# Performance work log

Measured on AMD Instinct MI355X. Metric: run time of the kernel, lower is better.

The kernel has to match this reference:

```python
import jax, jax.numpy as jnp
import numpy as np

H = 256      # hidden_channels
OUT = 128    # out_channels
NC = 20000   # central nodes
N1 = 60000   # child_cont nodes
N2 = 60000   # child_categ nodes
E = 200000   # edges per relation
B = 512      # graphs in batch
L = 2        # GNN layers
R = 4        # edge types


def seg_mean(vals, ids, n):
    s = jax.ops.segment_sum(vals, ids, num_segments=n)
    c = jax.ops.segment_sum(jnp.ones((vals.shape[0], 1), vals.dtype), ids, num_segments=n)
    return s / jnp.maximum(c, 1.0)


def setup_inputs() -> dict:
    key = jax.random.key(0)
    ks = jax.random.split(key, 24)
    nrm = lambda k, shp, s=1.0: jax.random.normal(k, shp, jnp.float32) * s

    def ei(k, ns, nd):
        k1, k2 = jax.random.split(k)
        return jnp.stack([jax.random.randint(k1, (E,), 0, ns, jnp.int32),
                          jax.random.randint(k2, (E,), 0, nd, jnp.int32)])

    inp = {
        'x_central': nrm(ks[0], (NC, 64)),
        'x_cont': nrm(ks[1], (N1, 16)),
        'x_categ': nrm(ks[2], (N2, 16)),
        'ei_c2cont': ei(ks[3], NC, N1),
        'ei_cont2c': ei(ks[4], N1, NC),
        'ei_c2categ': ei(ks[5], NC, N2),
        'ei_categ2c': ei(ks[6], N2, NC),
        'batch_central': jnp.sort(jax.random.randint(ks[7], (NC,), 0, B, jnp.int32)),
        'batch_cont': jnp.sort(jax.random.randint(ks[8], (N1,), 0, B, jnp.int32)),
        'batch_categ': jnp.sort(jax.random.randint(ks[9], (N2,), 0, B, jnp.int32)),
        'num_graphs': B,
        # input projections per node type
        'Wp_central': nrm(ks[10], (64, H), 1.0 / np.sqrt(64)),
        'bp_central': jnp.zeros((H,), jnp.float32),
        'Wp_cont': nrm(ks[11], (16, H), 0.25),
        'bp_cont': jnp.zeros((H,), jnp.float32),
        'Wp_categ': nrm(ks[12], (16, H), 0.25),
        'bp_categ': jnp.zeros((H,), jnp.float32),
        # per-layer, per-edge-type SAGEConv weights (to_hetero duplicates convs)
        'W_msg': nrm(ks[13], (L, R, H, H), 1.0 / np.sqrt(H)),
        'b_msg': jnp.zeros((L, R, H), jnp.float32),
        'W_root': nrm(ks[14], (L, R, H, H), 1.0 / np.sqrt(H)),
        # final graph linear
        'Wg': nrm(ks[15], (H, OUT), 1.0 / np.sqrt(H)),
        'bg': jnp.zeros((OUT,), jnp.float32),
    }
    return inp


def reference(x_central, x_cont, x_categ, ei_c2cont, ei_cont2c, ei_c2categ, ei_categ2c,
              batch_central, batch_cont, batch_categ, num_graphs,
              Wp_central, bp_central, Wp_cont, bp_cont, Wp_categ, bp_categ,
              W_msg, b_msg, W_root, Wg, bg):
    sizes = {'central': NC, 'child_cont': N1, 'child_categ': N2}
    x = {
        'central': x_central @ Wp_central + bp_central,
        'child_cont': x_cont @ Wp_cont + bp_cont,
        'child_categ': x_categ @ Wp_categ + bp_categ,
    }
    # (src_type, dst_type, edge_index, relation slot)
    rels = [
        ('central', 'child_cont', ei_c2cont, 0),
        ('child_cont', 'central', ei_cont2c, 1),
        ('central', 'child_categ', ei_c2categ, 2),
        ('child_categ', 'central', ei_categ2c, 3),
    ]
    n_layers = W_msg.shape[0]
    for l in range(n_layers):
        acc = {t: [] for t in x}
        for (st, dt, ei, r) in rels:
            src, dst = ei[0], ei[1]
            m = seg_mean(x[st][src], dst, sizes[dt])          # mean neighbor aggregation
            out = m @ W_msg[l, r] + b_msg[l, r] + x[dt] @ W_root[l, r]
            acc[dt].append(out)
        x = {t: jnp.mean(jnp.stack(acc[t], 0), 0) for t in acc}  # hetero aggr='mean'
        if l < n_layers - 1:
            x = {t: jax.nn.relu(v) for t, v in x.items()}
    # global mean pool per node type
    pooled = [
        seg_mean(x['central'], batch_central, num_graphs),
        seg_mean(x['child_cont'], batch_cont, num_graphs),
        seg_mean(x['child_categ'], batch_categ, num_graphs),
    ]
    graph_emb = jnp.mean(jnp.stack(pooled, 0), 0)  # 'stack' fusion
    return graph_emb @ Wg + bg
```

## Files before the change

### kernel.cpp

```cpp
#include <hip/hip_runtime.h>

#define Hh   256
#define NCn  20000
#define N1n  60000
#define N2n  60000
#define En   200000
#define Bn   512
#define OUTn 128
#define KA   96
#define PGW  1792

using bf16x8 = __attribute__((ext_vector_type(8))) __bf16;
using f32x4  = __attribute__((ext_vector_type(4))) float;
using f32x2  = __attribute__((ext_vector_type(2))) float;

__device__ __forceinline__ float bf2f(unsigned short u) {
    union { unsigned int i; float f; } v; v.i = ((unsigned int)u) << 16; return v.f;
}
__device__ __forceinline__ unsigned short f2bf(float f) {
    union { float f; unsigned int i; } v; v.f = f;
    unsigned int r = v.i + 0x7FFFu + ((v.i >> 16) & 1u);
    return (unsigned short)(r >> 16);
}
__device__ __forceinline__ int imax(int a, int b) { return a > b ? a : b; }

#if __has_builtin(__builtin_amdgcn_cvt_pk_fp8_f32) && __has_builtin(__builtin_amdgcn_cvt_pk_f32_fp8)
__device__ __forceinline__ unsigned int pack4_fp8(float v0, float v1, float v2, float v3) {
    int r = __builtin_amdgcn_cvt_pk_fp8_f32(v0, v1, 0, false);
    r = __builtin_amdgcn_cvt_pk_fp8_f32(v2, v3, r, true);
    return (unsigned int)r;
}
__device__ __forceinline__ void unpack4_fp8(unsigned int u, float& v0, float& v1, float& v2, float& v3) {
    f32x2 lo = __builtin_amdgcn_cvt_pk_f32_fp8((int)u, false);
    f32x2 hi = __builtin_amdgcn_cvt_pk_f32_fp8((int)u, true);
    v0 = lo[0]; v1 = lo[1]; v2 = hi[0]; v3 = hi[1];
}
#else
__device__ __forceinline__ unsigned char f32_to_fp8_1(float f) {
    union { float f; unsigned int i; } v; v.f = f;
    unsigned int s = (v.i >> 24) & 0x80u;
    float af = fabsf(f);
    if (!(af > 0.f)) return (unsigned char)s;
    if (af > 448.f) af = 448.f;
    v.f = af;
    int e = (int)((v.i >> 23) & 0xff) - 127;
    unsigned int m = v.i & 0x7fffffu;
    if (e < -9) return (unsigned char)s;
    if (e < -6) {
        int rb = 21 + (-6 - e) - 1;
        unsigned int man = 0x800000u | m;
        unsigned int keep = man >> (rb + 1);
        unsigned int rem = man & ((1u << (rb + 1)) - 1);
        unsigned int half = 1u << rb;
        keep += (rem > half) || (rem == half && (keep & 1));
        return (unsigned char)(s | keep);
    }
    unsigned int keep = m >> 20;
    unsigned int rem = m & 0xfffffu;
    keep += (rem > 0x80000u) || (rem == 0x80000u && (keep & 1));
    unsigned int ee = (unsigned int)(e + 7);
    if (keep == 8) { keep = 0; ee += 1; }
    if (ee >= 16) { ee = 15; keep = 6; }
    return (unsigned char)(s | (ee << 3) | keep);
}
__device__ __forceinline__ unsigned int pack4_fp8(float v0, float v1, float v2, float v3) {
    return (unsigned int)f32_to_fp8_1(v0) | ((unsigned int)f32_to_fp8_1(v1) << 8) |
           ((unsigned int)f32_to_fp8_1(v2) << 16) | ((unsigned int)f32_to_fp8_1(v3) << 24);
}
__device__ __forceinline__ float fp8_to_f32_1(unsigned int b) {
    unsigned int s = b >> 7, e = (b >> 3) & 15u, m = b & 7u;
    float v;
    if (e == 0) v = (float)m * (1.0f / 512.0f);
    else { union { unsigned int i; float f; } u; u.i = ((e + 120u) << 23) | (m << 20); v = u.f; }
    return s ? -v : v;
}
__device__ __forceinline__ void unpack4_fp8(unsigned int u, float& v0, float& v1, float& v2, float& v3) {
    v0 = fp8_to_f32_1(u & 0xffu); v1 = fp8_to_f32_1((u >> 8) & 0xffu);
    v2 = fp8_to_f32_1((u >> 16) & 0xffu); v3 = fp8_to_f32_1((u >> 24) & 0xffu);
}
#endif

struct CPtr4 { const int* p[4]; };
struct IPtr4 { int* p[4]; };
struct UPtr4 { uint2* p[4]; };

__device__ __forceinline__ float wpg_val(const float* Wm1, const float* Wr1, int k, int n) {
    int blk = k >> 8, kk = k & 255;
    float v;
    switch (blk) {
        case 0:  v = 0.5f * Wm1[1 * 65536 + kk * 256 + n]; break;
        case 1:  v = 0.5f * Wm1[3 * 65536 + kk * 256 + n]; break;
        case 2:  v = 0.5f * (Wr1[1 * 65536 + kk * 256 + n] + Wr1[3 * 65536 + kk * 256 + n]); break;
        case 3:  v = Wm1[0 * 65536 + kk * 256 + n]; break;
        case 4:  v = Wr1[0 * 65536 + kk * 256 + n]; break;
        case 5:  v = Wm1[2 * 65536 + kk * 256 + n]; break;
        default: v = Wr1[2 * 65536 + kk * 256 + n]; break;
    }
    return v * (1.0f / 3.0f);
}

#define QB0 6257
#define QB1 (QB0 + 288)
#define QB2 (QB1 + 896)
#define QB3 (QB2 + 3)
__global__ void __launch_bounds__(256) prep_mega(
        const float* __restrict__ xc, const float* __restrict__ x1, const float* __restrict__ x2,
        unsigned short* __restrict__ A0, unsigned short* __restrict__ A1,
        unsigned short* __restrict__ A2, unsigned short* __restrict__ A0c,
        unsigned short* __restrict__ xr1c, unsigned short* __restrict__ xr2c,
        int* __restrict__ deg_fill,
        const int* __restrict__ bc, const int* __restrict__ b1, const int* __restrict__ b2batch,
        int* __restrict__ bound,
        const float* __restrict__ Wm0, const float* __restrict__ Wr0,
        const float* __restrict__ bm0, const float* __restrict__ bpc,
        const float* __restrict__ bp1, const float* __restrict__ bp2,
        const float* __restrict__ Wpc, const float* __restrict__ Wp1, const float* __restrict__ Wp2,
        const float* __restrict__ Wm1, const float* __restrict__ Wr1,
        const float* __restrict__ bm1, const float* __restrict__ Wg, const float* __restrict__ bg,
        unsigned short* __restrict__ Wt3, unsigned short* __restrict__ W2t,
        float* __restrict__ bC, float* __restrict__ bB1, float* __restrict__ bB2,
        float* __restrict__ b2out) {
    __shared__ float smem[512];
    const int b = blockIdx.x, t = threadIdx.x;
    if (b < QB0) {
        const int c0 = NCn * 16, c1 = c0 + N1n * 8, c2 = c1 + N2n * 8;
        const int c3 = c2 + 320000, c4 = c3 + 3 * (Bn + 1);
        int idx = b * 256 + t;
        if (idx < c0) {
            int m = idx >> 4, c = (idx & 15) * 4;
            float4 v = *reinterpret_cast<const float4*>(xc + (size_t)m * 64 + c);
            ushort4 o = { f2bf(v.x), f2bf(v.y), f2bf(v.z), f2bf(v.w) };
            *reinterpret_cast<ushort4*>(A0 + (size_t)m * KA + c) = o;
            *reinterpret_cast<ushort4*>(A0c + (size_t)m * 64 + c) = o;
        } else if (idx < c2) {
            bool is1 = idx < c1;
            int i = idx - (is1 ? c0 : c1);
            int m = i >> 3, c = (i & 7) * 4;
            const float* x = is1 ? x1 : x2;
            unsigned short* A = is1 ? A1 : A2;
            unsigned short* xr = is1 ? xr1c : xr2c;
            ushort4 o = { 0, 0, 0, 0 };
            if (c < 16) {
                float4 v = *reinterpret_cast<const float4*>(x + (size_t)m * 16 + c);
                o.x = f2bf(v.x); o.y = f2bf(v.y); o.z = f2bf(v.z); o.w = f2bf(v.w);
                *reinterpret_cast<ushort4*>(xr + (size_t)m * 16 + c) = o;
            }
            *reinterpret_cast<ushort4*>(A + (size_t)m * KA + 64 + c) = o;
        } else if (idx < c3) {
            deg_fill[idx - c2] = 0;
        } else if (idx < c4) {
            int i4 = idx - c3;
            int ty = i4 / (Bn + 1); int bb = i4 - ty * (Bn + 1);
            const int* batch = (ty == 0) ? bc : (ty == 1) ? b1 : b2batch;
            int n = (ty == 0) ? NCn : (ty == 1) ? N1n : N2n;
            int lo = 0, hi = n;
            while (lo < hi) { int mid = (lo + hi) >> 1; if (batch[mid] < bb) lo = mid + 1; else hi = mid; }
            bound[i4] = lo;
        }
    } else if (b < QB1) {
        int bi = b - QB0;
        int mat = bi / 96, k = bi - mat * 96;
        int n = t;
        float acc = 0.f;
        if (k < 64) {
            const float* wp = Wpc + k * 256;
            if (mat == 0) {
#pragma unroll 8
                for (int j = 0; j < 256; ++j)
                    acc = fmaf(wp[j], 0.5f * (Wr0[1 * 65536 + j * 256 + n] + Wr0[3 * 65536 + j * 256 + n]), acc);
            } else if (mat == 1) {
#pragma unroll 8
                for (int j = 0; j < 256; ++j)
                    acc = fmaf(wp[j], Wm0[0 * 65536 + j * 256 + n], acc);
            } else {
#pragma unroll 8
                for (int j = 0; j < 256; ++j)
                    acc = fmaf(wp[j], Wm0[2 * 65536 + j * 256 + n], acc);
            }
        } else if (k < 80) {
            int kk = k - 64;
            if (mat == 0) {
                const float* wp = Wp1 + kk * 256;
#pragma unroll 8
                for (int j = 0; j < 256; ++j)
                    acc = fmaf(wp[j], 0.5f * Wm0[1 * 65536 + j * 256 + n], acc);
            } else if (mat == 1) {
                const float* wp = Wp1 + kk * 256;
#pragma unroll 8
                for (int j = 0; j < 256; ++j)
                    acc = fmaf(wp[j], Wr0[0 * 65536 + j * 256 + n], acc);
            } else {
                const float* wp = Wp2 + kk * 256;
#pragma unroll 8
                for (int j = 0; j < 256; ++j)
                    acc = fmaf(wp[j], Wr0[2 * 65536 + j * 256 + n], acc);
            }
        } else {
            if (mat == 0) {
                const float* wp = Wp2 + (k - 80) * 256;
#pragma unroll 8
                for (int j = 0; j < 256; ++j)
                    acc = fmaf(wp[j], 0.5f * Wm0[3 * 65536 + j * 256 + n], acc);
            }
        }
        Wt3[(size_t)mat * 256 * KA + n * KA + k] = f2bf(acc);
    } else if (b < QB2) {
        int kb = b - QB1;
        int k0 = kb * 2, k1 = k0 + 1;
        float* v0 = smem;
        float* v1 = smem + 256;
        v0[t] = wpg_val(Wm1, Wr1, k0, t);
        v1[t] = wpg_val(Wm1, Wr1, k1, t);
        __syncthreads();
        int o = t & 127;
        const float* vv = (t < 128) ? v0 : v1;
        int kk = (t < 128) ? k0 : k1;
        float acc = 0.f;
        for (int n = 0; n < 256; ++n) acc = fmaf(vv[n], Wg[n * OUTn + o], acc);
        W2t[(size_t)o * PGW + kk] = f2bf(acc);
    } else if (b < QB3) {
        int which = b - QB2;
        int n = t;
        if (which == 0) {
            float s0 = 0, s1 = 0, s2 = 0;
#pragma unroll 4
            for (int j = 0; j < 256; ++j) {
                float wr1 = Wr0[1 * 65536 + j * 256 + n], wr3 = Wr0[3 * 65536 + j * 256 + n];
                float wm1 = Wm0[1 * 65536 + j * 256 + n], wm3 = Wm0[3 * 65536 + j * 256 + n];
                s0 = fmaf(bpc[j], 0.5f * (wr1 + wr3), s0);
                s1 = fmaf(bp1[j], 0.5f * wm1, s1);
                s2 = fmaf(bp2[j], 0.5f * wm3, s2);
            }
            bC[n] = s0 + s1 + s2 + 0.5f * (bm0[1 * 256 + n] + bm0[3 * 256 + n]);
        } else if (which == 1) {
            float t0 = 0, t1 = 0;
#pragma unroll 4
            for (int j = 0; j < 256; ++j) {
                t0 = fmaf(bpc[j], Wm0[0 * 65536 + j * 256 + n], t0);
                t1 = fmaf(bp1[j], Wr0[0 * 65536 + j * 256 + n], t1);
            }
            bB1[n] = t0 + t1 + bm0[0 * 256 + n];
        } else {
            float u0 = 0, u1 = 0;
#pragma unroll 4
            for (int j = 0; j < 256; ++j) {
                u0 = fmaf(bpc[j], Wm0[2 * 65536 + j * 256 + n], u0);
                u1 = fmaf(bp2[j], Wr0[2 * 65536 + j * 256 + n], u1);
            }
            bB2[n] = u0 + u1 + bm0[2 * 256 + n];
        }
    } else {
        const float third = 1.0f / 3.0f;
        smem[t] = third * (0.5f * (bm1[1 * 256 + t] + bm1[3 * 256 + t]) +
                           bm1[0 * 256 + t] + bm1[2 * 256 + t]);
        __syncthreads();
        if (t < OUTn) {
            float acc = bg[t];
            for (int n = 0; n < 256; ++n) acc = fmaf(smem[n], Wg[n * OUTn + t], acc);
            b2out[t] = acc;
        }
    }
}

__device__ __forceinline__ int degoff_of(int rel) {
    const int t[4] = { 0, N1n, N1n + NCn, N1n + NCn + N2n };
    return t[rel];
}
__device__ __forceinline__ int nrel_of(int rel) {
    const int t[4] = { N1n, NCn, N2n, NCn };
    return t[rel];
}
__device__ __forceinline__ void rel_chunk(int b, int& rel, int& c) {
    if (b < 59)       { rel = 0; c = b; }
    else if (b < 79)  { rel = 1; c = b - 59; }
    else if (b < 138) { rel = 2; c = b - 79; }
    else              { rel = 3; c = b - 138; }
}
__global__ void deg_count_all(CPtr4 dst, int* __restrict__ deg_all) {
    int i = blockIdx.x * 256 + threadIdx.x;
    if (i >= 4 * En) return;
    int rel = i / En; int e = i - rel * En;
    atomicAdd(&deg_all[degoff_of(rel) + dst.p[rel][e]], 1);
}
__global__ void __launch_bounds__(1024) scan_chunk_all(const int* __restrict__ deg_all,
                                                       IPtr4 rp, int* __restrict__ partials) {
    int rel, c; rel_chunk(blockIdx.x, rel, c);
    int n = nrel_of(rel);
    __shared__ int sh[1024];
    int tid = threadIdx.x;
    int i = c * 1024 + tid;
    int v = (i < n) ? deg_all[degoff_of(rel) + i] : 0;
    sh[tid] = v; __syncthreads();
    for (int off = 1; off < 1024; off <<= 1) {
        int t = (tid >= off) ? sh[tid - off] : 0; __syncthreads();
        sh[tid] += t; __syncthreads();
    }
    if (i < n) rp.p[rel][i] = sh[tid] - v;
    if (tid == 1023) partials[rel * 64 + c] = sh[1023];
}
__global__ void scan_partials_all(int* partials) {
    const int nch[4] = { 59, 20, 59, 20 };
    int rel = blockIdx.x;
    __shared__ int sh[64];
    int tid = threadIdx.x;
    int v = (tid < nch[rel]) ? partials[rel * 64 + tid] : 0;
    sh[tid] = v; __syncthreads();
    for (int off = 1; off < 64; off <<= 1) {
        int t = (tid >= off) ? sh[tid - off] : 0; __syncthreads();
        sh[tid] += t; __syncthreads();
    }
    if (tid < nch[rel]) partials[rel * 64 + tid] = sh[tid] - v;
}
__global__ void __launch_bounds__(1024) scan_add_all(IPtr4 rp, const int* __restrict__ partials) {
    int rel, c; rel_chunk(blockIdx.x, rel, c);
    int n = nrel_of(rel);
    int tid = threadIdx.x;
    int i = c * 1024 + tid;
    if (i < n) rp.p[rel][i] += partials[rel * 64 + c];
    if (c == 0 && tid == 0) rp.p[rel][n] = En;
}
__global__ void scatter_all(CPtr4 src, CPtr4 dst, CPtr4 rp, int* fill_all, UPtr4 pay) {
    int i = blockIdx.x * 256 + threadIdx.x;
    if (i >= 4 * En) return;
    int rel = i / En; int e = i - rel * En;
    int d = dst.p[rel][e];
    int rb = rp.p[rel][d];
    int deg = rp.p[rel][d + 1] - rb;
    float w = 1.0f / (float)imax(deg, 1);
    int pos = rb + atomicAdd(&fill_all[degoff_of(rel) + d], 1);
    pay.p[rel][pos] = make_uint2((unsigned int)src.p[rel][e], __float_as_uint(w));
}

struct RawDesc {
    const unsigned short* feat;
    const int* rowptr;
    const uint2* pay;
    unsigned short* out;
    int fstride;
    int sh;
    int n_dst;
    int ocol;
};
__global__ void raw_agg(RawDesc d0, RawDesc d1, RawDesc d2, RawDesc d3) {
    RawDesc d = (blockIdx.y == 0) ? d0 : (blockIdx.y == 1) ? d1 : (blockIdx.y == 2) ? d2 : d3;
    int idx = blockIdx.x * 256 + threadIdx.x;
    int node = idx >> d.sh;
    int c4 = idx & ((1 << d.sh) - 1);
    if (node >= d.n_dst) return;
    int s = d.rowptr[node], e = d.rowptr[node + 1];
    float a0 = 0.f, a1 = 0.f, a2 = 0.f, a3 = 0.f;
    float b0 = 0.f, b1 = 0.f, b2 = 0.f, b3 = 0.f;
    int i = s;
    for (; i + 1 < e; i += 2) {
        int sc1 = (int)d.pay[i].x, sc2 = (int)d.pay[i + 1].x;
        ushort4 v1 = *reinterpret_cast<const ushort4*>(d.feat + (size_t)sc1 * d.fstride + c4 * 4);
        ushort4 v2 = *reinterpret_cast<const ushort4*>(d.feat + (size_t)sc2 * d.fstride + c4 * 4);
        a0 += bf2f(v1.x); a1 += bf2f(v1.y); a2 += bf2f(v1.z); a3 += bf2f(v1.w);
        b0 += bf2f(v2.x); b1 += bf2f(v2.y); b2 += bf2f(v2.z); b3 += bf2f(v2.w);
    }
    if (i < e) {
        int sc1 = (int)d.pay[i].x;
        ushort4 v1 = *reinterpret_cast<const ushort4*>(d.feat + (size_t)sc1 * d.fstride + c4 * 4);
        a0 += bf2f(v1.x); a1 += bf2f(v1.y); a2 += bf2f(v1.z); a3 += bf2f(v1.w);
    }
    a0 += b0; a1 += b1; a2 += b2; a3 += b3;
    float inv = 1.0f / (float)imax(e - s, 1);
    ushort4 o;
    o.x = f2bf(a0 * inv); o.y = f2bf(a1 * inv); o.z = f2bf(a2 * inv); o.w = f2bf(a3 * inv);
    *reinterpret_cast<ushort4*>(d.out + (size_t)node * KA + d.ocol + c4 * 4) = o;
}

struct G96 {
    const unsigned short* A;
    const unsigned short* Wt;
    const float* bias;
    unsigned char* C;
    int M;
};
__global__ void __launch_bounds__(256) gemm96(G96 g0, G96 g1, G96 g2) {
    G96 g = (blockIdx.y == 0) ? g0 : (blockIdx.y == 1) ? g1 : g2;
    const int m0 = blockIdx.x * 32;
    if (m0 >= g.M) return;
    const int tid = threadIdx.x;
    const int wid = tid >> 6, lane = tid & 63;
    const int llo = lane & 15, lhi = lane >> 4;
    const int cb = wid * 64;

    const unsigned short* pA[2];
#pragma unroll
    for (int rt = 0; rt < 2; ++rt)
        pA[rt] = g.A + (size_t)(m0 + rt * 16 + llo) * KA + lhi * 8;
    const unsigned short* pB[4];
#pragma unroll
    for (int ct = 0; ct < 4; ++ct)
        pB[ct] = g.Wt + (size_t)(cb + ct * 16 + llo) * KA + lhi * 8;

    f32x4 acc[2][4] = {};
    bf16x8 a0[2], a1[2], a2[2], b0[4], b1[4], b2[4];
#pragma unroll
    for (int t = 0; t < 2; ++t) {
        a0[t] = *reinterpret_cast<const bf16x8*>(pA[t]);
        a1[t] = *reinterpret_cast<const bf16x8*>(pA[t] + 32);
        a2[t] = *reinterpret_cast<const bf16x8*>(pA[t] + 64);
    }
#pragma unroll
    for (int t = 0; t < 4; ++t) {
        b0[t] = *reinterpret_cast<const bf16x8*>(pB[t]);
        b1[t] = *reinterpret_cast<const bf16x8*>(pB[t] + 32);
        b2[t] = *reinterpret_cast<const bf16x8*>(pB[t] + 64);
    }
#pragma unroll
    for (int rt = 0; rt < 2; ++rt)
#pragma unroll
        for (int ct = 0; ct < 4; ++ct) {
            acc[rt][ct] = __builtin_amdgcn_mfma_f32_16x16x32_bf16(b0[ct], a0[rt], acc[rt][ct], 0, 0, 0);
            acc[rt][ct] = __builtin_amdgcn_mfma_f32_16x16x32_bf16(b1[ct], a1[rt], acc[rt][ct], 0, 0, 0);
            acc[rt][ct] = __builtin_amdgcn_mfma_f32_16x16x32_bf16(b2[ct], a2[rt], acc[rt][ct], 0, 0, 0);
        }

#pragma unroll
    for (int rt = 0; rt < 2; ++rt) {
        const int row = m0 + rt * 16 + llo;
#pragma unroll
        for (int ct = 0; ct < 4; ++ct) {
            const int col0 = cb + ct * 16 + lhi * 4;
            float4 bv = *reinterpret_cast<const float4*>(g.bias + col0);
            float v0 = fmaxf(acc[rt][ct][0] + bv.x, 0.f);
            float v1 = fmaxf(acc[rt][ct][1] + bv.y, 0.f);
            float v2 = fmaxf(acc[rt][ct][2] + bv.z, 0.f);
            float v3 = fmaxf(acc[rt][ct][3] + bv.w, 0.f);
            unsigned int o = pack4_fp8(v0, v1, v2, v3);
            *reinterpret_cast<unsigned int*>(g.C + (size_t)row * 256 + col0) = o;
        }
    }
}

struct PDesc {
    const unsigned char* feat;
    const int* bound;
    const int* rowptr;
    const uint2* pay;
};
struct PAll { PDesc d[7]; };
__global__ void __launch_bounds__(256) pg_all(PAll all, float* __restrict__ part) {
    PDesc d = all.d[blockIdx.y];
    const int g = blockIdx.x, z = blockIdx.z;
    const int tid = threadIdx.x, wid = tid >> 6, lane = tid & 63;
    const int ns = d.bound[g], ne = d.bound[g + 1];
    float r0 = 0.f, r1 = 0.f, r2 = 0.f, r3 = 0.f;
    if (d.rowptr) {
        const int es = d.rowptr[ns], ee = d.rowptr[ne];
        const int len = ee - es;
        const int s = es + ((len * z) >> 2), e = es + ((len * (z + 1)) >> 2);
        float a[4][4] = {};
        for (int i = s + wid * 8; i < e; i += 32) {
            uint2 p[8]; float w[8];
#pragma unroll
            for (int j = 0; j < 8; ++j) {
                int ij = i + j;
                bool ok = ij < e;
                p[j] = d.pay[ok ? ij : (e - 1)];
                w[j] = ok ? __uint_as_float(p[j].y) : 0.f;
            }
            unsigned int u[8];
#pragma unroll
            for (int j = 0; j < 8; ++j)
                u[j] = *reinterpret_cast<const unsigned int*>(
                    d.feat + (size_t)p[j].x * 256 + lane * 4);
#pragma unroll
            for (int j = 0; j < 8; ++j) {
                float f0, f1, f2, f3;
                unpack4_fp8(u[j], f0, f1, f2, f3);
                int q = j & 3;
                a[q][0] = fmaf(f0, w[j], a[q][0]);
                a[q][1] = fmaf(f1, w[j], a[q][1]);
                a[q][2] = fmaf(f2, w[j], a[q][2]);
                a[q][3] = fmaf(f3, w[j], a[q][3]);
            }
        }
        r0 = (a[0][0] + a[1][0]) + (a[2][0] + a[3][0]);
        r1 = (a[0][1] + a[1][1]) + (a[2][1] + a[3][1]);
        r2 = (a[0][2] + a[1][2]) + (a[2][2] + a[3][2]);
        r3 = (a[0][3] + a[1][3]) + (a[2][3] + a[3][3]);
    } else {
        const int len = ne - ns;
        const int s = ns + ((len * z) >> 2), e = ns + ((len * (z + 1)) >> 2);
        float a[4][4] = {};
        for (int n = s + wid * 4; n < e; n += 16) {
            unsigned int u[4];
#pragma unroll
            for (int j = 0; j < 4; ++j) {
                int nj = n + j;
                bool ok = nj < e;
                u[j] = ok ? *reinterpret_cast<const unsigned int*>(
                                d.feat + (size_t)nj * 256 + lane * 4) : 0u;
            }
#pragma unroll
            for (int j = 0; j < 4; ++j) {
                float f0, f1, f2, f3;
                unpack4_fp8(u[j], f0, f1, f2, f3);
                a[j][0] += f0; a[j][1] += f1; a[j][2] += f2; a[j][3] += f3;
            }
        }
        r0 = (a[0][0] + a[1][0]) + (a[2][0] + a[3][0]);
        r1 = (a[0][1] + a[1][1]) + (a[2][1] + a[3][1]);
        r2 = (a[0][2] + a[1][2]) + (a[2][2] + a[3][2]);
        r3 = (a[0][3] + a[1][3]) + (a[2][3] + a[3][3]);
    }
    __shared__ float sh[4][256];
    sh[wid][lane * 4 + 0] = r0; sh[wid][lane * 4 + 1] = r1;
    sh[wid][lane * 4 + 2] = r2; sh[wid][lane * 4 + 3] = r3;
    __syncthreads();
    float r = (sh[0][tid] + sh[1][tid]) + (sh[2][tid] + sh[3][tid]);
    part[(size_t)((blockIdx.y * 4 + z) * Bn + g) * 256 + tid] = r;
}

__global__ void __launch_bounds__(256) final_direct(const float* __restrict__ part,
                                                    const int* __restrict__ bounds,
                                                    const unsigned short* __restrict__ W2t,
                                                    const float* __restrict__ b2,
                                                    float* __restrict__ out) {
    __shared__ float pgrow[PGW];
    __shared__ float red[256];
    const int btab[7] = { 0, 0, 0, 1, 1, 2, 2 };
    int g = blockIdx.x, t = threadIdx.x;
#pragma unroll
    for (int dsc = 0; dsc < 7; ++dsc) {
        const int* bb = bounds + btab[dsc] * (Bn + 1);
        int cnt = bb[g + 1] - bb[g];
        float s = 0.f;
#pragma unroll
        for (int z = 0; z < 4; ++z)
            s += part[(size_t)((dsc * 4 + z) * Bn + g) * 256 + t];
        pgrow[dsc * 256 + t] = s * (1.0f / (float)imax(cnt, 1));
    }
    __syncthreads();
    int o = t & 127, h = t >> 7;
    const unsigned short* wrow = W2t + (size_t)o * PGW + h * (PGW / 2);
    const float* prow = pgrow + h * (PGW / 2);
    float acc = 0.f;
    for (int k = 0; k < PGW / 2; k += 8) {
        ushort4 wa = *reinterpret_cast<const ushort4*>(wrow + k);
        ushort4 wb = *reinterpret_cast<const ushort4*>(wrow + k + 4);
        acc = fmaf(prow[k + 0], bf2f(wa.x), acc);
        acc = fmaf(prow[k + 1], bf2f(wa.y), acc);
        acc = fmaf(prow[k + 2], bf2f(wa.z), acc);
        acc = fmaf(prow[k + 3], bf2f(wa.w), acc);
        acc = fmaf(prow[k + 4], bf2f(wb.x), acc);
        acc = fmaf(prow[k + 5], bf2f(wb.y), acc);
        acc = fmaf(prow[k + 6], bf2f(wb.z), acc);
        acc = fmaf(prow[k + 7], bf2f(wb.w), acc);
    }
    red[t] = acc;
    __syncthreads();
    if (t < OUTn) out[(size_t)g * OUTn + t] = red[t] + red[t + 128] + b2[t];
}

extern "C" void kernel_launch(void* const* d_in, const int* in_sizes, int n_in,
                              void* d_out, int out_size, void* d_ws, size_t ws_size,
                              hipStream_t stream) {
    const float* x_central = (const float*)d_in[0];
    const float* x_cont    = (const float*)d_in[1];
    const float* x_categ   = (const float*)d_in[2];
    const int* ei_c2cont   = (const int*)d_in[3];
    const int* ei_cont2c   = (const int*)d_in[4];
    const int* ei_c2categ  = (const int*)d_in[5];
    const int* ei_categ2c  = (const int*)d_in[6];
    const int* batch_central = (const int*)d_in[7];
    const int* batch_cont    = (const int*)d_in[8];
    const int* batch_categ   = (const int*)d_in[9];
    const float* Wp_central = (const float*)d_in[11];
    const float* bp_central = (const float*)d_in[12];
    const float* Wp_cont    = (const float*)d_in[13];
    const float* bp_cont    = (const float*)d_in[14];
    const float* Wp_categ   = (const float*)d_in[15];
    const float* bp_categ   = (const float*)d_in[16];
    const float* W_msg  = (const float*)d_in[17];
    const float* b_msg  = (const float*)d_in[18];
    const float* W_root = (const float*)d_in[19];
    const float* Wg     = (const float*)d_in[20];
    const float* bg     = (const float*)d_in[21];
    float* out = (float*)d_out;

    char* base = (char*)d_ws;
    size_t off = 0;
    auto alloc = [&](size_t bytes) -> void* {
        off = (off + 255) & ~(size_t)255;
        void* p = base + off; off += bytes; return p;
    };

    unsigned short* A0   = (unsigned short*)alloc((size_t)NCn * KA * 2);
    unsigned short* A1   = (unsigned short*)alloc((size_t)N1n * KA * 2);
    unsigned short* A2   = (unsigned short*)alloc((size_t)N2n * KA * 2);
    unsigned short* A0c  = (unsigned short*)alloc((size_t)NCn * 64 * 2);
    unsigned short* xr1c = (unsigned short*)alloc((size_t)N1n * 16 * 2);
    unsigned short* xr2c = (unsigned short*)alloc((size_t)N2n * 16 * 2);
    unsigned char* hc1   = (unsigned char*)alloc((size_t)NCn * 256);
    unsigned char* h11   = (unsigned char*)alloc((size_t)N1n * 256);
    unsigned char* h21   = (unsigned char*)alloc((size_t)N2n * 256);
    float* part          = (float*)alloc((size_t)28 * Bn * 256 * 4);

    unsigned short* Wt3  = (unsigned short*)alloc((size_t)3 * 256 * KA * 2);
    unsigned short* W2t  = (unsigned short*)alloc((size_t)OUTn * PGW * 2);
    float* bC  = (float*)alloc(256 * 4);
    float* bB1 = (float*)alloc(256 * 4);
    float* bB2 = (float*)alloc(256 * 4);
    float* b2  = (float*)alloc(OUTn * 4);

    const int ndst[4] = { N1n, NCn, N2n, NCn };
    int* rp[4]; uint2* pay[4];
    for (int r = 0; r < 4; ++r) {
        rp[r]  = (int*)alloc((size_t)(ndst[r] + 1) * 4);
        pay[r] = (uint2*)alloc((size_t)En * 8);
    }
    int* deg_fill = (int*)alloc((size_t)320000 * 4);
    int* partials = (int*)alloc(256 * 4);
    int* bounds   = (int*)alloc((size_t)3 * (Bn + 1) * 4);
    (void)ws_size; (void)in_sizes; (void)n_in; (void)out_size;

    const float* Wm0 = W_msg;
    const float* Wr0 = W_root;
    const float* Wm1 = W_msg  + (size_t)4 * 65536;
    const float* Wr1 = W_root + (size_t)4 * 65536;
    const float* bm0 = b_msg;
    const float* bm1 = b_msg + 4 * 256;

    prep_mega<<<QB3 + 1, 256, 0, stream>>>(
        x_central, x_cont, x_categ, A0, A1, A2, A0c, xr1c, xr2c, deg_fill,
        batch_central, batch_cont, batch_categ, bounds,
        Wm0, Wr0, bm0, bp_central, bp_cont, bp_categ,
        Wp_central, Wp_cont, Wp_categ,
        Wm1, Wr1, bm1, Wg, bg,
        Wt3, W2t, bC, bB1, bB2, b2);

    CPtr4 srcs = {{ ei_c2cont, ei_cont2c, ei_c2categ, ei_categ2c }};
    CPtr4 dsts = {{ ei_c2cont + En, ei_cont2c + En, ei_c2categ + En, ei_categ2c + En }};
    IPtr4 rps  = {{ rp[0], rp[1], rp[2], rp[3] }};
    CPtr4 rpc  = {{ rp[0], rp[1], rp[2], rp[3] }};
    UPtr4 pys  = {{ pay[0], pay[1], pay[2], pay[3] }};
    deg_count_all<<<3125, 256, 0, stream>>>(dsts, deg_fill);
    scan_chunk_all<<<158, 1024, 0, stream>>>(deg_fill, rps, partials);
    scan_partials_all<<<4, 64, 0, stream>>>(partials);
    scan_add_all<<<158, 1024, 0, stream>>>(rps, partials);
    scatter_all<<<3125, 256, 0, stream>>>(srcs, dsts, rpc, deg_fill + 160000, pys);

    RawDesc r0 = { xr1c, rp[1], pay[1], A0, 16, 2, NCn, 64 };
    RawDesc r1 = { xr2c, rp[3], pay[3], A0, 16, 2, NCn, 80 };
    RawDesc r2 = { A0c,  rp[0], pay[0], A1, 64, 4, N1n, 0 };
    RawDesc r3 = { A0c,  rp[2], pay[2], A2, 64, 4, N2n, 0 };
    raw_agg<<<dim3(3750, 4), 256, 0, stream>>>(r0, r1, r2, r3);

    G96 gc = { A0, Wt3,                 bC,  hc1, NCn };
    G96 g1 = { A1, Wt3 + 1 * 256 * KA,  bB1, h11, N1n };
    G96 g2 = { A2, Wt3 + 2 * 256 * KA,  bB2, h21, N2n };
    gemm96<<<dim3(1875, 3), 256, 0, stream>>>(g1, g2, gc);

    PAll pa;
    pa.d[0] = { h11, bounds,                rp[1], pay[1] };
    pa.d[1] = { h21, bounds,                rp[3], pay[3] };
    pa.d[2] = { hc1, bounds,                nullptr, nullptr };
    pa.d[3] = { hc1, bounds + (Bn + 1),     rp[0], pay[0] };
    pa.d[4] = { h11, bounds + (Bn + 1),     nullptr, nullptr };
    pa.d[5] = { hc1, bounds + 2 * (Bn + 1), rp[2], pay[2] };
    pa.d[6] = { h21, bounds + 2 * (Bn + 1), nullptr, nullptr };
    pg_all<<<dim3(Bn, 7, 4), 256, 0, stream>>>(pa, part);

    final_direct<<<Bn, 256, 0, stream>>>(part, bounds, W2t, b2, out);
}
```

Measured before the change: 247.1 us.

## Make gemm96 persistent with A prefetch and loop pooling descriptors in-block

The gemm96 kernel moves from one block per 32-row tile to a grid-stride persistent loop over a fixed 625-block grid. Each block prefetches the next tile's A fragments while it runs the current MFMAs and epilogue, which amortises launch and wave startup and hides load latency. The pooling kernel drops its 7-descriptor grid dimension, so each block walks all seven descriptors in sequence with extra barriers. That cuts block count by 7x but serialises work per block, and the tile count uses M/32, which assumes M is a multiple of 32 (true for 20000 and 60000).

```diff
diff --git a/kernel.cpp b/kernel.cpp
--- a/kernel.cpp
+++ b/kernel.cpp
@@ -377,61 +377,78 @@
     unsigned char* C;
     int M;
 };
+#define G96_GRIDX 625
 __global__ void __launch_bounds__(256) gemm96(G96 g0, G96 g1, G96 g2) {
     G96 g = (blockIdx.y == 0) ? g0 : (blockIdx.y == 1) ? g1 : g2;
-    const int m0 = blockIdx.x * 32;
-    if (m0 >= g.M) return;
+    const int ntiles = g.M / 32;
+    int tile = blockIdx.x;
+    if (tile >= ntiles) return;
     const int tid = threadIdx.x;
     const int wid = tid >> 6, lane = tid & 63;
     const int llo = lane & 15, lhi = lane >> 4;
     const int cb = wid * 64;
 
-    const unsigned short* pA[2];
-#pragma unroll
-    for (int rt = 0; rt < 2; ++rt)
-        pA[rt] = g.A + (size_t)(m0 + rt * 16 + llo) * KA + lhi * 8;
     const unsigned short* pB[4];
 #pragma unroll
     for (int ct = 0; ct < 4; ++ct)
         pB[ct] = g.Wt + (size_t)(cb + ct * 16 + llo) * KA + lhi * 8;
-
-    f32x4 acc[2][4] = {};
-    bf16x8 a0[2], a1[2], a2[2], b0[4], b1[4], b2[4];
-#pragma unroll
-    for (int t = 0; t < 2; ++t) {
-        a0[t] = *reinterpret_cast<const bf16x8*>(pA[t]);
-        a1[t] = *reinterpret_cast<const bf16x8*>(pA[t] + 32);
-        a2[t] = *reinterpret_cast<const bf16x8*>(pA[t] + 64);
-    }
-#pragma unroll
-    for (int t = 0; t < 4; ++t) {
-        b0[t] = *reinterpret_cast<const bf16x8*>(pB[t]);
-        b1[t] = *reinterpret_cast<const bf16x8*>(pB[t] + 32);
-        b2[t] = *reinterpret_cast<const bf16x8*>(pB[t] + 64);
-    }
-#pragma unroll
-    for (int rt = 0; rt < 2; ++rt)
-#pragma unroll
-        for (int ct = 0; ct < 4; ++ct) {
-            acc[rt][ct] = __builtin_amdgcn_mfma_f32_16x16x32_bf16(b0[ct], a0[rt], acc[rt][ct], 0, 0, 0);
-            acc[rt][ct] = __builtin_amdgcn_mfma_f32_16x16x32_bf16(b1[ct], a1[rt], acc[rt][ct], 0, 0, 0);
-            acc[rt][ct] = __builtin_amdgcn_mfma_f32_16x16x32_bf16(b2[ct], a2[rt], acc[rt][ct], 0, 0, 0);
-        }
-
-#pragma unroll
-    for (int rt = 0; rt < 2; ++rt) {
-        const int row = m0 + rt * 16 + llo;
-#pragma unroll
-        for (int ct = 0; ct < 4; ++ct) {
-            const int col0 = cb + ct * 16 + lhi * 4;
-            float4 bv = *reinterpret_cast<const float4*>(g.bias + col0);
-            float v0 = fmaxf(acc[rt][ct][0] + bv.x, 0.f);
-            float v1 = fmaxf(acc[rt][ct][1] + bv.y, 0.f);
-            float v2 = fmaxf(acc[rt][ct][2] + bv.z, 0.f);
-            float v3 = fmaxf(acc[rt][ct][3] + bv.w, 0.f);
-            unsigned int o = pack4_fp8(v0, v1, v2, v3);
-            *reinterpret_cast<unsigned int*>(g.C + (size_t)row * 256 + col0) = o;
-        }
+    const size_t aoff = (size_t)llo * KA + lhi * 8;
+
+    bf16x8 aCur[3][2], aNxt[3][2];
+    auto loadA = [&](bf16x8 (&A)[3][2], int t0) {
+        const unsigned short* base = g.A + (size_t)t0 * 32 * KA + aoff;
+#pragma unroll
+        for (int rt = 0; rt < 2; ++rt) {
+            const unsigned short* p = base + (size_t)rt * 16 * KA;
+            A[0][rt] = *reinterpret_cast<const bf16x8*>(p);
+            A[1][rt] = *reinterpret_cast<const bf16x8*>(p + 32);
+            A[2][rt] = *reinterpret_cast<const bf16x8*>(p + 64);
+        }
+    };
+    loadA(aCur, tile);
+
+    for (; tile < ntiles; tile += G96_GRIDX) {
+        const int nt = tile + G96_GRIDX;
+        bf16x8 b0[4], b1[4], b2[4];
+#pragma unroll
+        for (int t = 0; t < 4; ++t) {
+            b0[t] = *reinterpret_cast<const bf16x8*>(pB[t]);
+            b1[t] = *reinterpret_cast<const bf16x8*>(pB[t] + 32);
+            b2[t] = *reinterpret_cast<const bf16x8*>(pB[t] + 64);
+        }
+        if (nt < ntiles) loadA(aNxt, nt);
+
+        f32x4 acc[2][4] = {};
+#pragma unroll
+        for (int rt = 0; rt < 2; ++rt)
+#pragma unroll
+            for (int ct = 0; ct < 4; ++ct) {
+                acc[rt][ct] = __builtin_amdgcn_mfma_f32_16x16x32_bf16(b0[ct], aCur[0][rt], acc[rt][ct], 0, 0, 0);
+                acc[rt][ct] = __builtin_amdgcn_mfma_f32_16x16x32_bf16(b1[ct], aCur[1][rt], acc[rt][ct], 0, 0, 0);
+                acc[rt][ct] = __builtin_amdgcn_mfma_f32_16x16x32_bf16(b2[ct], aCur[2][rt], acc[rt][ct], 0, 0, 0);
+            }
+
+        const int m0 = tile * 32;
+#pragma unroll
+        for (int rt = 0; rt < 2; ++rt) {
+            const int row = m0 + rt * 16 + llo;
+#pragma unroll
+            for (int ct = 0; ct < 4; ++ct) {
+                const int col0 = cb + ct * 16 + lhi * 4;
+                float4 bv = *reinterpret_cast<const float4*>(g.bias + col0);
+                float v0 = fmaxf(acc[rt][ct][0] + bv.x, 0.f);
+                float v1 = fmaxf(acc[rt][ct][1] + bv.y, 0.f);
+                float v2 = fmaxf(acc[rt][ct][2] + bv.z, 0.f);
+                float v3 = fmaxf(acc[rt][ct][3] + bv.w, 0.f);
+                unsigned int o = pack4_fp8(v0, v1, v2, v3);
+                *reinterpret_cast<unsigned int*>(g.C + (size_t)row * 256 + col0) = o;
+            }
+        }
+#pragma unroll
+        for (int ks = 0; ks < 3; ++ks)
+#pragma unroll
+            for (int rt = 0; rt < 2; ++rt)
+                aCur[ks][rt] = aNxt[ks][rt];
     }
 }
 
@@ -443,76 +460,79 @@
 };
 struct PAll { PDesc d[7]; };
 __global__ void __launch_bounds__(256) pg_all(PAll all, float* __restrict__ part) {
-    PDesc d = all.d[blockIdx.y];
-    const int g = blockIdx.x, z = blockIdx.z;
+    const int g = blockIdx.x, z = blockIdx.y;
     const int tid = threadIdx.x, wid = tid >> 6, lane = tid & 63;
-    const int ns = d.bound[g], ne = d.bound[g + 1];
-    float r0 = 0.f, r1 = 0.f, r2 = 0.f, r3 = 0.f;
-    if (d.rowptr) {
-        const int es = d.rowptr[ns], ee = d.rowptr[ne];
-        const int len = ee - es;
-        const int s = es + ((len * z) >> 2), e = es + ((len * (z + 1)) >> 2);
-        float a[4][4] = {};
-        for (int i = s + wid * 8; i < e; i += 32) {
-            uint2 p[8]; float w[8];
-#pragma unroll
-            for (int j = 0; j < 8; ++j) {
-                int ij = i + j;
-                bool ok = ij < e;
-                p[j] = d.pay[ok ? ij : (e - 1)];
-                w[j] = ok ? __uint_as_float(p[j].y) : 0.f;
-            }
-            unsigned int u[8];
-#pragma unroll
-            for (int j = 0; j < 8; ++j)
-                u[j] = *reinterpret_cast<const unsigned int*>(
-                    d.feat + (size_t)p[j].x * 256 + lane * 4);
-#pragma unroll
-            for (int j = 0; j < 8; ++j) {
-                float f0, f1, f2, f3;
-                unpack4_fp8(u[j], f0, f1, f2, f3);
-                int q = j & 3;
-                a[q][0] = fmaf(f0, w[j], a[q][0]);
-                a[q][1] = fmaf(f1, w[j], a[q][1]);
-                a[q][2] = fmaf(f2, w[j], a[q][2]);
-                a[q][3] = fmaf(f3, w[j], a[q][3]);
-            }
-        }
-        r0 = (a[0][0] + a[1][0]) + (a[2][0] + a[3][0]);
-        r1 = (a[0][1] + a[1][1]) + (a[2][1] + a[3][1]);
-        r2 = (a[0][2] + a[1][2]) + (a[2][2] + a[3][2]);
-        r3 = (a[0][3] + a[1][3]) + (a[2][3] + a[3][3]);
-    } else {
-        const int len = ne - ns;
-        const int s = ns + ((len * z) >> 2), e = ns + ((len * (z + 1)) >> 2);
-        float a[4][4] = {};
-        for (int n = s + wid * 4; n < e; n += 16) {
-            unsigned int u[4];
-#pragma unroll
-            for (int j = 0; j < 4; ++j) {
-                int nj = n + j;
-                bool ok = nj < e;
-                u[j] = ok ? *reinterpret_cast<const unsigned int*>(
-                                d.feat + (size_t)nj * 256 + lane * 4) : 0u;
-            }
-#pragma unroll
-            for (int j = 0; j < 4; ++j) {
-                float f0, f1, f2, f3;
-                unpack4_fp8(u[j], f0, f1, f2, f3);
-                a[j][0] += f0; a[j][1] += f1; a[j][2] += f2; a[j][3] += f3;
-            }
-        }
-        r0 = (a[0][0] + a[1][0]) + (a[2][0] + a[3][0]);
-        r1 = (a[0][1] + a[1][1]) + (a[2][1] + a[3][1]);
-        r2 = (a[0][2] + a[1][2]) + (a[2][2] + a[3][2]);
-        r3 = (a[0][3] + a[1][3]) + (a[2][3] + a[3][3]);
-    }
     __shared__ float sh[4][256];
-    sh[wid][lane * 4 + 0] = r0; sh[wid][lane * 4 + 1] = r1;
-    sh[wid][lane * 4 + 2] = r2; sh[wid][lane * 4 + 3] = r3;
-    __syncthreads();
-    float r = (sh[0][tid] + sh[1][tid]) + (sh[2][tid] + sh[3][tid]);
-    part[(size_t)((blockIdx.y * 4 + z) * Bn + g) * 256 + tid] = r;
+    for (int dsc = 0; dsc < 7; ++dsc) {
+        PDesc d = all.d[dsc];
+        const int ns = d.bound[g], ne = d.bound[g + 1];
+        float r0 = 0.f, r1 = 0.f, r2 = 0.f, r3 = 0.f;
+        if (d.rowptr) {
+            const int es = d.rowptr[ns], ee = d.rowptr[ne];
+            const int len = ee - es;
+            const int s = es + ((len * z) >> 2), e = es + ((len * (z + 1)) >> 2);
+            float a[4][4] = {};
+            for (int i = s + wid * 8; i < e; i += 32) {
+                uint2 p[8]; float w[8];
+#pragma unroll
+                for (int j = 0; j < 8; ++j) {
+                    int ij = i + j;
+                    bool ok = ij < e;
+                    p[j] = d.pay[ok ? ij : (e - 1)];
+                    w[j] = ok ? __uint_as_float(p[j].y) : 0.f;
+                }
+                unsigned int u[8];
+#pragma unroll
+                for (int j = 0; j < 8; ++j)
+                    u[j] = *reinterpret_cast<const unsigned int*>(
+                        d.feat + (size_t)p[j].x * 256 + lane * 4);
+#pragma unroll
+                for (int j = 0; j < 8; ++j) {
+                    float f0, f1, f2, f3;
+                    unpack4_fp8(u[j], f0, f1, f2, f3);
+                    int q = j & 3;
+                    a[q][0] = fmaf(f0, w[j], a[q][0]);
+                    a[q][1] = fmaf(f1, w[j], a[q][1]);
+                    a[q][2] = fmaf(f2, w[j], a[q][2]);
+                    a[q][3] = fmaf(f3, w[j], a[q][3]);
+                }
+            }
+            r0 = (a[0][0] + a[1][0]) + (a[2][0] + a[3][0]);
+            r1 = (a[0][1] + a[1][1]) + (a[2][1] + a[3][1]);
+            r2 = (a[0][2] + a[1][2]) + (a[2][2] + a[3][2]);
+            r3 = (a[0][3] + a[1][3]) + (a[2][3] + a[3][3]);
+        } else {
+            const int len = ne - ns;
+            const int s = ns + ((len * z) >> 2), e = ns + ((len * (z + 1)) >> 2);
+            float a[4][4] = {};
+            for (int n = s + wid * 4; n < e; n += 16) {
+                unsigned int u[4];
+#pragma unroll
+                for (int j = 0; j < 4; ++j) {
+                    int nj = n + j;
+                    bool ok = nj < e;
+                    u[j] = ok ? *reinterpret_cast<const unsigned int*>(
+                                    d.feat + (size_t)nj * 256 + lane * 4) : 0u;
+                }
+#pragma unroll
+                for (int j = 0; j < 4; ++j) {
+                    float f0, f1, f2, f3;
+                    unpack4_fp8(u[j], f0, f1, f2, f3);
+                    a[j][0] += f0; a[j][1] += f1; a[j][2] += f2; a[j][3] += f3;
+                }
+            }
+            r0 = (a[0][0] + a[1][0]) + (a[2][0] + a[3][0]);
+            r1 = (a[0][1] + a[1][1]) + (a[2][1] + a[3][1]);
+            r2 = (a[0][2] + a[1][2]) + (a[2][2] + a[3][2]);
+            r3 = (a[0][3] + a[1][3]) + (a[2][3] + a[3][3]);
+        }
+        sh[wid][lane * 4 + 0] = r0; sh[wid][lane * 4 + 1] = r1;
+        sh[wid][lane * 4 + 2] = r2; sh[wid][lane * 4 + 3] = r3;
+        __syncthreads();
+        float r = (sh[0][tid] + sh[1][tid]) + (sh[2][tid] + sh[3][tid]);
+        part[(size_t)((dsc * 4 + z) * Bn + g) * 256 + tid] = r;
+        __syncthreads();
+    }
 }
 
 __global__ void __launch_bounds__(256) final_direct(const float* __restrict__ part,
@@ -653,7 +673,7 @@
     G96 gc = { A0, Wt3,                 bC,  hc1, NCn };
     G96 g1 = { A1, Wt3 + 1 * 256 * KA,  bB1, h11, N1n };
     G96 g2 = { A2, Wt3 + 2 * 256 * KA,  bB2, h21, N2n };
-    gemm96<<<dim3(1875, 3), 256, 0, stream>>>(g1, g2, gc);
+    gemm96<<<dim3(G96_GRIDX, 3), 256, 0, stream>>>(g1, g2, gc);
 
     PAll pa;
     pa.d[0] = { h11, bounds,                rp[1], pay[1] };
@@ -663,7 +683,7 @@
     pa.d[4] = { h11, bounds + (Bn + 1),     nullptr, nullptr };
     pa.d[5] = { hc1, bounds + 2 * (Bn + 1), rp[2], pay[2] };
     pa.d[6] = { h21, bounds + 2 * (Bn + 1), nullptr, nullptr };
-    pg_all<<<dim3(Bn, 7, 4), 256, 0, stream>>>(pa, part);
+    pg_all<<<dim3(Bn, 4), 256, 0, stream>>>(pa, part);
 
     final_direct<<<Bn, 256, 0, stream>>>(part, bounds, W2t, b2, out);
 }
```

Measured after the change: 258.7 us. 4.7% more time.
